# Optimization experiments

Measured on AMD Instinct MI355X. Metric: run time of the kernel, lower is better.

The kernel has to match this reference:

```python
import jax, jax.numpy as jnp
import numpy as np

L = 2          # num_layers
H = 1024       # hidden_size
E = 1024       # embedding_size (== H, required by the feedback matmul)
T = 64         # len(list_desc) decision steps


def setup_inputs() -> dict:
    key = jax.random.key(0)
    ks = jax.random.split(key, 6)
    s = 1.0 / np.sqrt(H)  # keep LSTM gates out of saturation
    return {
        "W_ih": jax.random.normal(ks[0], (L, 4 * H, H), jnp.float32) * s,
        "W_hh": jax.random.normal(ks[1], (L, 4 * H, H), jnp.float32) * s,
        "b_ih": jax.random.normal(ks[2], (L, 4 * H), jnp.float32) * s,
        "b_hh": jax.random.normal(ks[3], (L, 4 * H), jnp.float32) * s,
        "We": jax.random.normal(ks[4], (T, E, H), jnp.float32) * s,
        "be": jax.random.normal(ks[5], (T, E), jnp.float32) * s,
    }


def _lstm_multilayer_step(x, h, c, W_ih, W_hh, b_ih, b_hh):
    # x: [1, E]; h, c: [L, 1, H].  PyTorch gate order: i, f, g, o.
    hs, cs = [], []
    inp = x
    for l in range(L):  # small fixed layer loop
        gates = inp @ W_ih[l].T + b_ih[l] + h[l] @ W_hh[l].T + b_hh[l]  # [1, 4H]
        i, f, g, o = jnp.split(gates, 4, axis=-1)
        c_new = jax.nn.sigmoid(f) * c[l] + jax.nn.sigmoid(i) * jnp.tanh(g)
        h_new = jax.nn.sigmoid(o) * jnp.tanh(c_new)
        hs.append(h_new)
        cs.append(c_new)
        inp = h_new
    return jnp.stack(hs), jnp.stack(cs), inp  # inp = top-layer hidden [1, H]


def reference(W_ih, W_hh, b_ih, b_hh, We, be):
    x0 = jnp.zeros((1, E), jnp.float32)
    h0 = jnp.zeros((L, 1, H), jnp.float32)
    c0 = jnp.zeros((L, 1, H), jnp.float32)

    def step(carry, per_step):
        x, h, c = carry
        We_t, be_t = per_step  # [E, H], [E]
        h, c, top = _lstm_multilayer_step(x, h, c, W_ih, W_hh, b_ih, b_hh)
        logits = top @ We_t.T + be_t            # [1, E]
        decision = jax.nn.softmax(logits, -1)    # [1, E]
        x_next = decision @ We_t                 # [1, H] == [1, E]
        return (x_next, h, c), decision

    _, decisions = jax.lax.scan(step, (x0, h0, c0), (We, be))
    return decisions[:, 0, :]  # [T, E] concatenated decisions
```

## Files before the change

### kernel.cpp

```cpp
#include <hip/hip_runtime.h>

static constexpr int L_ = 2;
static constexpr int H_ = 1024;
static constexpr int E_ = 1024;
static constexpr int T_ = 64;
static constexpr int NB = 256;
static constexpr int BT = 1024;

static constexpr int WS_XV = 0;
static constexpr int WS_H  = WS_XV + (T_ + 1) * H_;
static constexpr int WS_LG = WS_H + T_ * L_ * H_;
static constexpr size_t WS_BYTES = (size_t)(WS_LG + T_ * E_) * 4;

static constexpr unsigned SENT = 0xFFFFFFFFu;

__device__ __forceinline__ float sigm(float v) { return 1.0f / (1.0f + expf(-v)); }

__device__ __forceinline__ unsigned cload_u(const float* p) {
  return __hip_atomic_load((const unsigned*)p, __ATOMIC_RELAXED, __HIP_MEMORY_SCOPE_AGENT);
}
__device__ __forceinline__ void cstore(float* p, float v) {
  __hip_atomic_store(p, v, __ATOMIC_RELAXED, __HIP_MEMORY_SCOPE_AGENT);
}
__device__ __forceinline__ float poll1(const float* p) {
  unsigned v = cload_u(p);
  while (v == SENT) { __builtin_amdgcn_s_sleep(1); v = cload_u(p); }
  return __uint_as_float(v);
}

__global__ __launch_bounds__(BT, 4) void ctrl_kernel(
    const float* __restrict__ W_ih, const float* __restrict__ W_hh,
    const float* __restrict__ b_ih, const float* __restrict__ b_hh,
    const float* __restrict__ We,   const float* __restrict__ be,
    float* __restrict__ out, float* __restrict__ ws)
{
  const int tid  = threadIdx.x;
  const int b    = blockIdx.x;
  const int lane = tid & 63;
  const int w    = tid >> 6;
  const int wl   = w >> 3;
  const int wq   = (w >> 1) & 3;
  const int wh   = w & 1;

  float* xv = ws + WS_XV;
  float* hh = ws + WS_H;
  float* lg = ws + WS_LG;

  const int cswz = ((b & 7) * 32 + (b >> 3)) * 4;

  __shared__ float  s_x[H_];
  __shared__ float  s_h[H_];
  __shared__ float  s_h1[H_];
  __shared__ float  s_gd[2][4][2][4];
  __shared__ float  s_bias[2][4][4];
  __shared__ float  s_c[2][4];
  __shared__ float  s_red[16];
  __shared__ float  s_redm[16];
  __shared__ float  s_reds[16];
  __shared__ float4 s_part4[16];

  if (tid < 32) {
    const int l = tid >> 4, q = (tid >> 2) & 3, u = tid & 3;
    const int j = b * 4 + u;
    s_bias[l][q][u] = b_ih[(size_t)l * 4 * H_ + q * H_ + j]
                    + b_hh[(size_t)l * 4 * H_ + q * H_ + j];
  }
  if (tid < 8) s_c[tid >> 2][tid & 3] = 0.0f;

  float4 wr[4][4];
  {
    const float* Wbase = (wh == 0) ? W_ih : W_hh;
    #pragma unroll
    for (int u = 0; u < 4; ++u) {
      const size_t row = (size_t)wl * 4 * H_ * H_
                       + ((size_t)wq * H_ + (size_t)(b * 4 + u)) * (size_t)H_;
      #pragma unroll
      for (int m = 0; m < 4; ++m)
        wr[u][m] = *(const float4*)&Wbase[row + (size_t)m * 256 + lane * 4];
    }
  }
  #pragma unroll
  for (int u = 0; u < 4; ++u)
    #pragma unroll
    for (int m = 0; m < 4; ++m)
      asm volatile("" : "+v"(wr[u][m].x), "+v"(wr[u][m].y),
                        "+v"(wr[u][m].z), "+v"(wr[u][m].w));

  for (int t = 0; t < T_; ++t) {
    const float* We_t = We + (size_t)t * E_ * H_;
    const float* be_t = be + (size_t)t * E_;

    const float4 wlog = *(const float4*)&We_t[((size_t)(b * 4 + (tid >> 8))) * H_ + (tid & 255) * 4];
    const float4 wfb  = *(const float4*)&We_t[(size_t)tid * H_ + cswz];

    if (t == 0) {
      s_x[tid] = 0.0f; s_h[tid] = 0.0f; s_h1[tid] = 0.0f;
    } else {
      const float* px = &xv[(size_t)t * H_ + tid];
      const float* ph = &hh[((size_t)(t - 1) * L_ + 0) * H_ + tid];
      const float* pk = &hh[((size_t)(t - 1) * L_ + 1) * H_ + tid];
      unsigned vx = cload_u(px), vh = cload_u(ph), vk = cload_u(pk);
      while (vx == SENT) { __builtin_amdgcn_s_sleep(1); vx = cload_u(px); }
      while (vh == SENT) { __builtin_amdgcn_s_sleep(1); vh = cload_u(ph); }
      while (vk == SENT) { __builtin_amdgcn_s_sleep(1); vk = cload_u(pk); }
      s_x[tid] = __uint_as_float(vx);
      s_h[tid] = __uint_as_float(vh);
      s_h1[tid] = __uint_as_float(vk);
    }
    __syncthreads();
    if (wl == 0 || wh == 1) {
      const float4* vin = (wl == 0) ? ((wh == 0) ? (const float4*)s_x : (const float4*)s_h)
                                    : (const float4*)s_h1;
      float a0 = 0.f, a1 = 0.f, a2 = 0.f, a3 = 0.f;
      #pragma unroll
      for (int m = 0; m < 4; ++m) {
        const float4 x4 = vin[m * 64 + lane];
        a0 += wr[0][m].x * x4.x + wr[0][m].y * x4.y + wr[0][m].z * x4.z + wr[0][m].w * x4.w;
        a1 += wr[1][m].x * x4.x + wr[1][m].y * x4.y + wr[1][m].z * x4.z + wr[1][m].w * x4.w;
        a2 += wr[2][m].x * x4.x + wr[2][m].y * x4.y + wr[2][m].z * x4.z + wr[2][m].w * x4.w;
        a3 += wr[3][m].x * x4.x + wr[3][m].y * x4.y + wr[3][m].z * x4.z + wr[3][m].w * x4.w;
      }
      #pragma unroll
      for (int off = 32; off; off >>= 1) {
        a0 += __shfl_down(a0, off, 64);
        a1 += __shfl_down(a1, off, 64);
        a2 += __shfl_down(a2, off, 64);
        a3 += __shfl_down(a3, off, 64);
      }
      if (lane == 0) {
        s_gd[wl][wq][wh][0] = a0; s_gd[wl][wq][wh][1] = a1;
        s_gd[wl][wq][wh][2] = a2; s_gd[wl][wq][wh][3] = a3;
      }
    }
    __syncthreads();
    if (tid < 4) {
      const int u = tid;
      const float g0 = s_gd[0][0][0][u] + s_gd[0][0][1][u] + s_bias[0][0][u];
      const float g1 = s_gd[0][1][0][u] + s_gd[0][1][1][u] + s_bias[0][1][u];
      const float g2 = s_gd[0][2][0][u] + s_gd[0][2][1][u] + s_bias[0][2][u];
      const float g3 = s_gd[0][3][0][u] + s_gd[0][3][1][u] + s_bias[0][3][u];
      const float cn = sigm(g1) * s_c[0][u] + sigm(g0) * tanhf(g2);
      s_c[0][u] = cn;
      cstore(&hh[((size_t)t * L_ + 0) * H_ + b * 4 + u], sigm(g3) * tanhf(cn));
    }

    s_x[tid] = poll1(&hh[((size_t)t * L_ + 0) * H_ + tid]);
    __syncthreads();
    if (wl == 1 && wh == 0) {
      const float4* vin = (const float4*)s_x;
      float a0 = 0.f, a1 = 0.f, a2 = 0.f, a3 = 0.f;
      #pragma unroll
      for (int m = 0; m < 4; ++m) {
        const float4 x4 = vin[m * 64 + lane];
        a0 += wr[0][m].x * x4.x + wr[0][m].y * x4.y + wr[0][m].z * x4.z + wr[0][m].w * x4.w;
        a1 += wr[1][m].x * x4.x + wr[1][m].y * x4.y + wr[1][m].z * x4.z + wr[1][m].w * x4.w;
        a2 += wr[2][m].x * x4.x + wr[2][m].y * x4.y + wr[2][m].z * x4.z + wr[2][m].w * x4.w;
        a3 += wr[3][m].x * x4.x + wr[3][m].y * x4.y + wr[3][m].z * x4.z + wr[3][m].w * x4.w;
      }
      #pragma unroll
      for (int off = 32; off; off >>= 1) {
        a0 += __shfl_down(a0, off, 64);
        a1 += __shfl_down(a1, off, 64);
        a2 += __shfl_down(a2, off, 64);
        a3 += __shfl_down(a3, off, 64);
      }
      if (lane == 0) {
        s_gd[1][wq][0][0] = a0; s_gd[1][wq][0][1] = a1;
        s_gd[1][wq][0][2] = a2; s_gd[1][wq][0][3] = a3;
      }
    }
    __syncthreads();
    if (tid < 4) {
      const int u = tid;
      const float g0 = s_gd[1][0][0][u] + s_gd[1][0][1][u] + s_bias[1][0][u];
      const float g1 = s_gd[1][1][0][u] + s_gd[1][1][1][u] + s_bias[1][1][u];
      const float g2 = s_gd[1][2][0][u] + s_gd[1][2][1][u] + s_bias[1][2][u];
      const float g3 = s_gd[1][3][0][u] + s_gd[1][3][1][u] + s_bias[1][3][u];
      const float cn = sigm(g1) * s_c[1][u] + sigm(g0) * tanhf(g2);
      s_c[1][u] = cn;
      cstore(&hh[((size_t)t * L_ + 1) * H_ + b * 4 + u], sigm(g3) * tanhf(cn));
    }

    s_x[tid] = poll1(&hh[((size_t)t * L_ + 1) * H_ + tid]);
    __syncthreads();
    {
      const int rr = tid >> 8;
      const float4 h4 = ((const float4*)s_x)[tid & 255];
      float a = wlog.x * h4.x + wlog.y * h4.y + wlog.z * h4.z + wlog.w * h4.w;
      #pragma unroll
      for (int off = 32; off; off >>= 1) a += __shfl_down(a, off, 64);
      if (lane == 0) s_red[w] = a;
      __syncthreads();
      if ((tid & 255) == 0) {
        const int e = b * 4 + rr;
        cstore(&lg[(size_t)t * E_ + e],
               s_red[rr * 4] + s_red[rr * 4 + 1] + s_red[rr * 4 + 2]
             + s_red[rr * 4 + 3] + be_t[e]);
      }
    }

    {
      s_x[tid] = poll1(&lg[(size_t)t * E_ + tid]);
      __syncthreads();
      const float v = s_x[tid];
      float mm = v;
      #pragma unroll
      for (int off = 32; off; off >>= 1) mm = fmaxf(mm, __shfl_down(mm, off, 64));
      if (lane == 0) s_redm[w] = mm;
      __syncthreads();
      mm = s_redm[0];
      #pragma unroll
      for (int k = 1; k < 16; ++k) mm = fmaxf(mm, s_redm[k]);
      const float ev = expf(v - mm);
      float sv = ev;
      #pragma unroll
      for (int off = 32; off; off >>= 1) sv += __shfl_down(sv, off, 64);
      if (lane == 0) s_reds[w] = sv;
      __syncthreads();
      float ssum = 0.f;
      #pragma unroll
      for (int k = 0; k < 16; ++k) ssum += s_reds[k];
      const float inv = 1.0f / ssum;
      const float d = ev * inv;

      if ((tid >> 2) == b) out[(size_t)t * E_ + tid] = d;

      float4 acc = make_float4(d * wfb.x, d * wfb.y, d * wfb.z, d * wfb.w);
      #pragma unroll
      for (int off = 32; off; off >>= 1) {
        acc.x += __shfl_down(acc.x, off, 64);
        acc.y += __shfl_down(acc.y, off, 64);
        acc.z += __shfl_down(acc.z, off, 64);
        acc.w += __shfl_down(acc.w, off, 64);
      }
      if (lane == 0) s_part4[w] = acc;
      __syncthreads();
      if (tid < 4) {
        float s = 0.f;
        #pragma unroll
        for (int k = 0; k < 16; ++k)
          s += ((const float*)&s_part4[k])[tid];
        cstore(&xv[(size_t)(t + 1) * H_ + cswz + tid], s);
      }
    }
  }
}

extern "C" void kernel_launch(void* const* d_in, const int* in_sizes, int n_in,
                              void* d_out, int out_size, void* d_ws, size_t ws_size,
                              hipStream_t stream) {
  const float* W_ih = (const float*)d_in[0];
  const float* W_hh = (const float*)d_in[1];
  const float* b_ih = (const float*)d_in[2];
  const float* b_hh = (const float*)d_in[3];
  const float* We   = (const float*)d_in[4];
  const float* be   = (const float*)d_in[5];
  float* out = (float*)d_out;
  float* ws  = (float*)d_ws;

  (void)hipMemsetAsync(ws, 0xFF, WS_BYTES, stream);

  void* args[] = {(void*)&W_ih, (void*)&W_hh, (void*)&b_ih, (void*)&b_hh,
                  (void*)&We,   (void*)&be,   (void*)&out,  (void*)&ws};
  (void)hipLaunchCooperativeKernel((const void*)ctrl_kernel, dim3(NB), dim3(BT),
                                   args, 0, stream);
}
```

Measured before the change: 1.228 ms.

## Replace per-element sentinel polling with per-block flag arrays polled by one wave

Instead of every thread spinning on its own data element until the sentinel clears, each producer block now sets a per-block flag after its stores drain (s_waitcnt vmcnt(0)), and a single wave polls 256 flags with a wave-wide all-reduction before the block reads the data. The We_t row loads are moved after the layer-0 store so they overlap with waiting, and the per-step bias values are preloaded into shared memory. This is meant to cut global polling traffic and latency across grid-wide handoffs. Correctness now depends on flag stores becoming visible only after the data stores, which relies on relaxed atomics plus the vmcnt wait rather than release/acquire ordering.

After: 1.834 ms. 1.49x slower.

```diff
diff --git a/kernel.cpp b/kernel.cpp
--- a/kernel.cpp
+++ b/kernel.cpp
@@ -10,22 +10,38 @@
 static constexpr int WS_XV = 0;
 static constexpr int WS_H  = WS_XV + (T_ + 1) * H_;
 static constexpr int WS_LG = WS_H + T_ * L_ * H_;
-static constexpr size_t WS_BYTES = (size_t)(WS_LG + T_ * E_) * 4;
+static constexpr int WS_F0 = WS_LG + T_ * E_;
+static constexpr int WS_F1 = WS_F0 + T_ * NB;
+static constexpr int WS_F2 = WS_F1 + T_ * NB;
+static constexpr int WS_F3 = WS_F2 + T_ * NB;
+static constexpr size_t WS_BYTES = (size_t)(WS_F3 + (T_ + 1) * NB) * 4;
 
 static constexpr unsigned SENT = 0xFFFFFFFFu;
 
 __device__ __forceinline__ float sigm(float v) { return 1.0f / (1.0f + expf(-v)); }
 
-__device__ __forceinline__ unsigned cload_u(const float* p) {
-  return __hip_atomic_load((const unsigned*)p, __ATOMIC_RELAXED, __HIP_MEMORY_SCOPE_AGENT);
+__device__ __forceinline__ float cload(const float* p) {
+  return __hip_atomic_load(p, __ATOMIC_RELAXED, __HIP_MEMORY_SCOPE_AGENT);
 }
 __device__ __forceinline__ void cstore(float* p, float v) {
   __hip_atomic_store(p, v, __ATOMIC_RELAXED, __HIP_MEMORY_SCOPE_AGENT);
 }
-__device__ __forceinline__ float poll1(const float* p) {
-  unsigned v = cload_u(p);
-  while (v == SENT) { __builtin_amdgcn_s_sleep(1); v = cload_u(p); }
-  return __uint_as_float(v);
+__device__ __forceinline__ unsigned cloadu(const unsigned* p) {
+  return __hip_atomic_load(p, __ATOMIC_RELAXED, __HIP_MEMORY_SCOPE_AGENT);
+}
+__device__ __forceinline__ void cstoreu(unsigned* p, unsigned v) {
+  __hip_atomic_store(p, v, __ATOMIC_RELAXED, __HIP_MEMORY_SCOPE_AGENT);
+}
+
+__device__ __forceinline__ void wait256(const unsigned* f) {
+  const int lane = threadIdx.x & 63;
+  const unsigned* p = f + lane * 4;
+  for (;;) {
+    const unsigned a = cloadu(p + 0), b = cloadu(p + 1),
+                   c = cloadu(p + 2), d = cloadu(p + 3);
+    const bool ok = (a != SENT) & (b != SENT) & (c != SENT) & (d != SENT);
+    if (__all(ok)) break;
+  }
 }
 
 __global__ __launch_bounds__(BT, 4) void ctrl_kernel(
@@ -42,9 +58,14 @@
   const int wq   = (w >> 1) & 3;
   const int wh   = w & 1;
 
-  float* xv = ws + WS_XV;
-  float* hh = ws + WS_H;
-  float* lg = ws + WS_LG;
+  float*    xv  = ws + WS_XV;
+  float*    hh  = ws + WS_H;
+  float*    lg  = ws + WS_LG;
+  unsigned* wsu = (unsigned*)ws;
+  unsigned* fh0 = wsu + WS_F0;
+  unsigned* fh1 = wsu + WS_F1;
+  unsigned* flg = wsu + WS_F2;
+  unsigned* fxv = wsu + WS_F3;
 
   const int cswz = ((b & 7) * 32 + (b >> 3)) * 4;
 
@@ -53,6 +74,7 @@
   __shared__ float  s_h1[H_];
   __shared__ float  s_gd[2][4][2][4];
   __shared__ float  s_bias[2][4][4];
+  __shared__ float  s_be[T_ * 4];
   __shared__ float  s_c[2][4];
   __shared__ float  s_red[16];
   __shared__ float  s_redm[16];
@@ -66,6 +88,8 @@
                     + b_hh[(size_t)l * 4 * H_ + q * H_ + j];
   }
   if (tid < 8) s_c[tid >> 2][tid & 3] = 0.0f;
+  if (tid < T_ * 4)
+    s_be[tid] = be[(size_t)(tid >> 2) * E_ + b * 4 + (tid & 3)];
 
   float4 wr[4][4];
   {
@@ -88,24 +112,15 @@
 
   for (int t = 0; t < T_; ++t) {
     const float* We_t = We + (size_t)t * E_ * H_;
-    const float* be_t = be + (size_t)t * E_;
-
-    const float4 wlog = *(const float4*)&We_t[((size_t)(b * 4 + (tid >> 8))) * H_ + (tid & 255) * 4];
-    const float4 wfb  = *(const float4*)&We_t[(size_t)tid * H_ + cswz];
 
     if (t == 0) {
       s_x[tid] = 0.0f; s_h[tid] = 0.0f; s_h1[tid] = 0.0f;
     } else {
-      const float* px = &xv[(size_t)t * H_ + tid];
-      const float* ph = &hh[((size_t)(t - 1) * L_ + 0) * H_ + tid];
-      const float* pk = &hh[((size_t)(t - 1) * L_ + 1) * H_ + tid];
-      unsigned vx = cload_u(px), vh = cload_u(ph), vk = cload_u(pk);
-      while (vx == SENT) { __builtin_amdgcn_s_sleep(1); vx = cload_u(px); }
-      while (vh == SENT) { __builtin_amdgcn_s_sleep(1); vh = cload_u(ph); }
-      while (vk == SENT) { __builtin_amdgcn_s_sleep(1); vk = cload_u(pk); }
-      s_x[tid] = __uint_as_float(vx);
-      s_h[tid] = __uint_as_float(vh);
-      s_h1[tid] = __uint_as_float(vk);
+      if (w == 15) wait256(fxv + (size_t)t * NB);
+      __syncthreads();
+      s_x[tid]  = cload(&xv[(size_t)t * H_ + tid]);
+      s_h[tid]  = cload(&hh[((size_t)(t - 1) * L_ + 0) * H_ + tid]);
+      s_h1[tid] = cload(&hh[((size_t)(t - 1) * L_ + 1) * H_ + tid]);
     }
     __syncthreads();
     if (wl == 0 || wh == 1) {
@@ -143,8 +158,17 @@
       s_c[0][u] = cn;
       cstore(&hh[((size_t)t * L_ + 0) * H_ + b * 4 + u], sigm(g3) * tanhf(cn));
     }
-
-    s_x[tid] = poll1(&hh[((size_t)t * L_ + 0) * H_ + tid]);
+    if (w == 0) {
+      asm volatile("s_waitcnt vmcnt(0)" ::: "memory");
+      if (lane == 0) cstoreu(fh0 + (size_t)t * NB + b, 1u);
+    }
+
+    const float4 wlog = *(const float4*)&We_t[((size_t)(b * 4 + (tid >> 8))) * H_ + (tid & 255) * 4];
+    const float4 wfb  = *(const float4*)&We_t[(size_t)tid * H_ + cswz];
+
+    if (w == 15) wait256(fh0 + (size_t)t * NB);
+    __syncthreads();
+    s_x[tid] = cload(&hh[((size_t)t * L_ + 0) * H_ + tid]);
     __syncthreads();
     if (wl == 1 && wh == 0) {
       const float4* vin = (const float4*)s_x;
@@ -180,28 +204,38 @@
       s_c[1][u] = cn;
       cstore(&hh[((size_t)t * L_ + 1) * H_ + b * 4 + u], sigm(g3) * tanhf(cn));
     }
-
-    s_x[tid] = poll1(&hh[((size_t)t * L_ + 1) * H_ + tid]);
+    if (w == 0) {
+      asm volatile("s_waitcnt vmcnt(0)" ::: "memory");
+      if (lane == 0) cstoreu(fh1 + (size_t)t * NB + b, 1u);
+    }
+
+    if (w == 15) wait256(fh1 + (size_t)t * NB);
+    __syncthreads();
+    s_x[tid] = cload(&hh[((size_t)t * L_ + 1) * H_ + tid]);
     __syncthreads();
     {
-      const int rr = tid >> 8;
       const float4 h4 = ((const float4*)s_x)[tid & 255];
       float a = wlog.x * h4.x + wlog.y * h4.y + wlog.z * h4.z + wlog.w * h4.w;
       #pragma unroll
       for (int off = 32; off; off >>= 1) a += __shfl_down(a, off, 64);
       if (lane == 0) s_red[w] = a;
-      __syncthreads();
-      if ((tid & 255) == 0) {
-        const int e = b * 4 + rr;
-        cstore(&lg[(size_t)t * E_ + e],
-               s_red[rr * 4] + s_red[rr * 4 + 1] + s_red[rr * 4 + 2]
-             + s_red[rr * 4 + 3] + be_t[e]);
-      }
-    }
-
+    }
+    __syncthreads();
+    if (tid < 4) {
+      const float v = s_red[tid * 4] + s_red[tid * 4 + 1] + s_red[tid * 4 + 2]
+                    + s_red[tid * 4 + 3] + s_be[t * 4 + tid];
+      cstore(&lg[(size_t)t * E_ + b * 4 + tid], v);
+    }
+    if (w == 0) {
+      asm volatile("s_waitcnt vmcnt(0)" ::: "memory");
+      if (lane == 0) cstoreu(flg + (size_t)t * NB + b, 1u);
+    }
+
+    if (w == 15) wait256(flg + (size_t)t * NB);
+    __syncthreads();
+    s_x[tid] = cload(&lg[(size_t)t * E_ + tid]);
+    __syncthreads();
     {
-      s_x[tid] = poll1(&lg[(size_t)t * E_ + tid]);
-      __syncthreads();
       const float v = s_x[tid];
       float mm = v;
       #pragma unroll
@@ -241,6 +275,10 @@
         for (int k = 0; k < 16; ++k)
           s += ((const float*)&s_part4[k])[tid];
         cstore(&xv[(size_t)(t + 1) * H_ + cswz + tid], s);
+      }
+      if (w == 0) {
+        asm volatile("s_waitcnt vmcnt(0)" ::: "memory");
+        if (lane == 0) cstoreu(fxv + (size_t)(t + 1) * NB + b, 1u);
       }
     }
   }
```

## Compute recurrent matvecs early from local h and prefetch next-step We

Applied to the files above, without the earlier changes.

Each step's W_hh products are now computed as soon as the matching hidden state is already in shared memory (layer-0 W_hh right after h0 is broadcast, layer-1 W_hh alongside the logits). This removes the extra polling of previous-step h vectors at the start of each step and drops two shared buffers. The We rows for step t+1 are loaded at the end of step t, so the fetch overlaps the grid-wide wait, and the be slices are cached in shared memory. The reordering relies on s_gd partials persisting correctly across steps, which is why s_gd is zero-initialized.

Result: faster. 992.0 us, median of 3 (-19.2%).

```diff
diff --git a/kernel.cpp b/kernel.cpp
--- a/kernel.cpp
+++ b/kernel.cpp
@@ -16,15 +16,15 @@
 
 __device__ __forceinline__ float sigm(float v) { return 1.0f / (1.0f + expf(-v)); }
 
-__device__ __forceinline__ unsigned cload_u(const float* p) {
+__device__ __forceinline__ unsigned cloadu(const float* p) {
   return __hip_atomic_load((const unsigned*)p, __ATOMIC_RELAXED, __HIP_MEMORY_SCOPE_AGENT);
 }
 __device__ __forceinline__ void cstore(float* p, float v) {
   __hip_atomic_store(p, v, __ATOMIC_RELAXED, __HIP_MEMORY_SCOPE_AGENT);
 }
 __device__ __forceinline__ float poll1(const float* p) {
-  unsigned v = cload_u(p);
-  while (v == SENT) { __builtin_amdgcn_s_sleep(1); v = cload_u(p); }
+  unsigned v = cloadu(p);
+  while (v == SENT) { __builtin_amdgcn_s_sleep(1); v = cloadu(p); }
   return __uint_as_float(v);
 }
 
@@ -49,10 +49,9 @@
   const int cswz = ((b & 7) * 32 + (b >> 3)) * 4;
 
   __shared__ float  s_x[H_];
-  __shared__ float  s_h[H_];
-  __shared__ float  s_h1[H_];
   __shared__ float  s_gd[2][4][2][4];
   __shared__ float  s_bias[2][4][4];
+  __shared__ float  s_be[T_ * 4];
   __shared__ float  s_c[2][4];
   __shared__ float  s_red[16];
   __shared__ float  s_redm[16];
@@ -66,6 +65,9 @@
                     + b_hh[(size_t)l * 4 * H_ + q * H_ + j];
   }
   if (tid < 8) s_c[tid >> 2][tid & 3] = 0.0f;
+  if (tid < 64) ((float*)s_gd)[tid] = 0.0f;
+  if (tid < T_ * 4)
+    s_be[tid] = be[(size_t)(tid >> 2) * E_ + b * 4 + (tid & 3)];
 
   float4 wr[4][4];
   {
@@ -86,52 +88,37 @@
       asm volatile("" : "+v"(wr[u][m].x), "+v"(wr[u][m].y),
                         "+v"(wr[u][m].z), "+v"(wr[u][m].w));
 
+  auto dot_to = [&](const float4* vin, int dl, int dq, int dh) {
+    float a0 = 0.f, a1 = 0.f, a2 = 0.f, a3 = 0.f;
+    #pragma unroll
+    for (int m = 0; m < 4; ++m) {
+      const float4 x4 = vin[m * 64 + lane];
+      a0 += wr[0][m].x * x4.x + wr[0][m].y * x4.y + wr[0][m].z * x4.z + wr[0][m].w * x4.w;
+      a1 += wr[1][m].x * x4.x + wr[1][m].y * x4.y + wr[1][m].z * x4.z + wr[1][m].w * x4.w;
+      a2 += wr[2][m].x * x4.x + wr[2][m].y * x4.y + wr[2][m].z * x4.z + wr[2][m].w * x4.w;
+      a3 += wr[3][m].x * x4.x + wr[3][m].y * x4.y + wr[3][m].z * x4.z + wr[3][m].w * x4.w;
+    }
+    #pragma unroll
+    for (int off = 32; off; off >>= 1) {
+      a0 += __shfl_down(a0, off, 64);
+      a1 += __shfl_down(a1, off, 64);
+      a2 += __shfl_down(a2, off, 64);
+      a3 += __shfl_down(a3, off, 64);
+    }
+    if (lane == 0) {
+      s_gd[dl][dq][dh][0] = a0; s_gd[dl][dq][dh][1] = a1;
+      s_gd[dl][dq][dh][2] = a2; s_gd[dl][dq][dh][3] = a3;
+    }
+  };
+
+  float4 wlog = *(const float4*)&We[((size_t)(b * 4 + (tid >> 8))) * H_ + (tid & 255) * 4];
+  float4 wfb  = *(const float4*)&We[(size_t)tid * H_ + cswz];
+
   for (int t = 0; t < T_; ++t) {
-    const float* We_t = We + (size_t)t * E_ * H_;
-    const float* be_t = be + (size_t)t * E_;
-
-    const float4 wlog = *(const float4*)&We_t[((size_t)(b * 4 + (tid >> 8))) * H_ + (tid & 255) * 4];
-    const float4 wfb  = *(const float4*)&We_t[(size_t)tid * H_ + cswz];
-
-    if (t == 0) {
-      s_x[tid] = 0.0f; s_h[tid] = 0.0f; s_h1[tid] = 0.0f;
-    } else {
-      const float* px = &xv[(size_t)t * H_ + tid];
-      const float* ph = &hh[((size_t)(t - 1) * L_ + 0) * H_ + tid];
-      const float* pk = &hh[((size_t)(t - 1) * L_ + 1) * H_ + tid];
-      unsigned vx = cload_u(px), vh = cload_u(ph), vk = cload_u(pk);
-      while (vx == SENT) { __builtin_amdgcn_s_sleep(1); vx = cload_u(px); }
-      while (vh == SENT) { __builtin_amdgcn_s_sleep(1); vh = cload_u(ph); }
-      while (vk == SENT) { __builtin_amdgcn_s_sleep(1); vk = cload_u(pk); }
-      s_x[tid] = __uint_as_float(vx);
-      s_h[tid] = __uint_as_float(vh);
-      s_h1[tid] = __uint_as_float(vk);
-    }
-    __syncthreads();
-    if (wl == 0 || wh == 1) {
-      const float4* vin = (wl == 0) ? ((wh == 0) ? (const float4*)s_x : (const float4*)s_h)
-                                    : (const float4*)s_h1;
-      float a0 = 0.f, a1 = 0.f, a2 = 0.f, a3 = 0.f;
-      #pragma unroll
-      for (int m = 0; m < 4; ++m) {
-        const float4 x4 = vin[m * 64 + lane];
-        a0 += wr[0][m].x * x4.x + wr[0][m].y * x4.y + wr[0][m].z * x4.z + wr[0][m].w * x4.w;
-        a1 += wr[1][m].x * x4.x + wr[1][m].y * x4.y + wr[1][m].z * x4.z + wr[1][m].w * x4.w;
-        a2 += wr[2][m].x * x4.x + wr[2][m].y * x4.y + wr[2][m].z * x4.z + wr[2][m].w * x4.w;
-        a3 += wr[3][m].x * x4.x + wr[3][m].y * x4.y + wr[3][m].z * x4.z + wr[3][m].w * x4.w;
-      }
-      #pragma unroll
-      for (int off = 32; off; off >>= 1) {
-        a0 += __shfl_down(a0, off, 64);
-        a1 += __shfl_down(a1, off, 64);
-        a2 += __shfl_down(a2, off, 64);
-        a3 += __shfl_down(a3, off, 64);
-      }
-      if (lane == 0) {
-        s_gd[wl][wq][wh][0] = a0; s_gd[wl][wq][wh][1] = a1;
-        s_gd[wl][wq][wh][2] = a2; s_gd[wl][wq][wh][3] = a3;
-      }
-    }
+    if (t == 0) s_x[tid] = 0.0f;
+    else        s_x[tid] = poll1(&xv[(size_t)t * H_ + tid]);
+    __syncthreads();
+    if (wl == 0 && wh == 0) dot_to((const float4*)s_x, 0, wq, 0);
     __syncthreads();
     if (tid < 4) {
       const int u = tid;
@@ -146,29 +133,8 @@
 
     s_x[tid] = poll1(&hh[((size_t)t * L_ + 0) * H_ + tid]);
     __syncthreads();
-    if (wl == 1 && wh == 0) {
-      const float4* vin = (const float4*)s_x;
-      float a0 = 0.f, a1 = 0.f, a2 = 0.f, a3 = 0.f;
-      #pragma unroll
-      for (int m = 0; m < 4; ++m) {
-        const float4 x4 = vin[m * 64 + lane];
-        a0 += wr[0][m].x * x4.x + wr[0][m].y * x4.y + wr[0][m].z * x4.z + wr[0][m].w * x4.w;
-        a1 += wr[1][m].x * x4.x + wr[1][m].y * x4.y + wr[1][m].z * x4.z + wr[1][m].w * x4.w;
-        a2 += wr[2][m].x * x4.x + wr[2][m].y * x4.y + wr[2][m].z * x4.z + wr[2][m].w * x4.w;
-        a3 += wr[3][m].x * x4.x + wr[3][m].y * x4.y + wr[3][m].z * x4.z + wr[3][m].w * x4.w;
-      }
-      #pragma unroll
-      for (int off = 32; off; off >>= 1) {
-        a0 += __shfl_down(a0, off, 64);
-        a1 += __shfl_down(a1, off, 64);
-        a2 += __shfl_down(a2, off, 64);
-        a3 += __shfl_down(a3, off, 64);
-      }
-      if (lane == 0) {
-        s_gd[1][wq][0][0] = a0; s_gd[1][wq][0][1] = a1;
-        s_gd[1][wq][0][2] = a2; s_gd[1][wq][0][3] = a3;
-      }
-    }
+    if (wl == 1 && wh == 0) dot_to((const float4*)s_x, 1, wq, 0);
+    if (wl == 0 && wh == 1) dot_to((const float4*)s_x, 0, wq, 1);
     __syncthreads();
     if (tid < 4) {
       const int u = tid;
@@ -184,24 +150,23 @@
     s_x[tid] = poll1(&hh[((size_t)t * L_ + 1) * H_ + tid]);
     __syncthreads();
     {
-      const int rr = tid >> 8;
       const float4 h4 = ((const float4*)s_x)[tid & 255];
       float a = wlog.x * h4.x + wlog.y * h4.y + wlog.z * h4.z + wlog.w * h4.w;
       #pragma unroll
       for (int off = 32; off; off >>= 1) a += __shfl_down(a, off, 64);
       if (lane == 0) s_red[w] = a;
-      __syncthreads();
-      if ((tid & 255) == 0) {
-        const int e = b * 4 + rr;
-        cstore(&lg[(size_t)t * E_ + e],
-               s_red[rr * 4] + s_red[rr * 4 + 1] + s_red[rr * 4 + 2]
-             + s_red[rr * 4 + 3] + be_t[e]);
-      }
-    }
-
+    }
+    if (wl == 1 && wh == 1) dot_to((const float4*)s_x, 1, wq, 1);
+    __syncthreads();
+    if (tid < 4) {
+      const float v = s_red[tid * 4] + s_red[tid * 4 + 1] + s_red[tid * 4 + 2]
+                    + s_red[tid * 4 + 3] + s_be[t * 4 + tid];
+      cstore(&lg[(size_t)t * E_ + b * 4 + tid], v);
+    }
+
+    s_x[tid] = poll1(&lg[(size_t)t * E_ + tid]);
+    __syncthreads();
     {
-      s_x[tid] = poll1(&lg[(size_t)t * E_ + tid]);
-      __syncthreads();
       const float v = s_x[tid];
       float mm = v;
       #pragma unroll
@@ -243,6 +208,12 @@
         cstore(&xv[(size_t)(t + 1) * H_ + cswz + tid], s);
       }
     }
+
+    if (t + 1 < T_) {
+      const float* Wn = We + (size_t)(t + 1) * E_ * H_;
+      wlog = *(const float4*)&Wn[((size_t)(b * 4 + (tid >> 8))) * H_ + (tid & 255) * 4];
+      wfb  = *(const float4*)&Wn[(size_t)tid * H_ + cswz];
+    }
   }
 }
 
```
